# Optimization experiments

Measured on AMD Instinct MI355X. Metric: run time of the kernel, lower is better.

## Reference

```python
import jax, jax.numpy as jnp
import numpy as np

B, S, D, H = 2, 2048, 1024, 16
HD = D // H
SPARSITY = 0.1
LAMBDA_MAX = 10.0
ALPHA = 5.0


def local_prior_mask(seq_len: int, sparsity: float) -> jnp.ndarray:
    # |i - j| <= window_size // 2, window_size = int(seq_len * sparsity)
    window_size = max(1, int(seq_len * sparsity))
    rows = jnp.arange(seq_len)[:, None]
    cols = jnp.arange(seq_len)[None, :]
    return jnp.abs(rows - cols) <= (window_size // 2)


def setup_inputs() -> dict:
    key = jax.random.key(0)
    ks = jax.random.split(key, 12)
    scale = 1.0 / np.sqrt(D)
    inp = {
        'x': jax.random.normal(ks[0], (B, S, D), dtype=jnp.float32),
        'u_prev': jax.random.uniform(ks[1], (B, 1), dtype=jnp.float32),
        'Wq': jax.random.normal(ks[2], (D, D), dtype=jnp.float32) * scale,
        'bq': jnp.zeros((D,), dtype=jnp.float32),
        'Wk': jax.random.normal(ks[3], (D, D), dtype=jnp.float32) * scale,
        'bk': jnp.zeros((D,), dtype=jnp.float32),
        'Wv': jax.random.normal(ks[4], (D, D), dtype=jnp.float32) * scale,
        'bv': jnp.zeros((D,), dtype=jnp.float32),
        'Wo': jax.random.normal(ks[5], (D, D), dtype=jnp.float32) * scale,
        'bo': jnp.zeros((D,), dtype=jnp.float32),
    }
    return inp


def reference(x, u_prev, Wq, bq, Wk, bk, Wv, bv, Wo, bo):
    b, s, _ = x.shape
    # projections (torch Linear: y = x W^T + b)
    def proj(W, bias):
        return (x @ W.T + bias).reshape(b, s, H, HD).transpose(0, 2, 1, 3)  # [B,H,S,HD]
    q = proj(Wq, bq)
    k = proj(Wk, bk)
    v = proj(Wv, bv)

    # dynamic gating: lambda = lambda_max * exp(-alpha * u_prev), shape [B,1,1,1]
    lam = (LAMBDA_MAX * jnp.exp(-ALPHA * u_prev)).reshape(b, 1, 1, 1)

    prior = local_prior_mask(s, SPARSITY)  # [S,S] bool

    scores = jnp.einsum('bhqd,bhkd->bhqk', q, k) / jnp.sqrt(jnp.asarray(HD, x.dtype))
    # additive prior bias: penalize positions outside the structural prior by -lambda
    scores = scores - lam * (~prior).astype(x.dtype)

    attn = jax.nn.softmax(scores, axis=-1)
    out = jnp.einsum('bhqk,bhkd->bhqd', attn, v)           # [B,H,S,HD]
    out = out.transpose(0, 2, 1, 3).reshape(b, s, D)        # [B,S,D]
    out = out @ Wo.T + bo
    return out, lam.reshape(b, 1)
```

## Files before the change

### kernel.cpp

```cpp
#include <hip/hip_runtime.h>

typedef __attribute__((ext_vector_type(8))) short short8;
typedef __attribute__((ext_vector_type(4))) float f32x4;

#define MFMA16(a,b,c) __builtin_amdgcn_mfma_f32_16x16x32_bf16(a,b,c,0,0,0)

__device__ __forceinline__ unsigned short f2bf(float f){
  unsigned int u = __float_as_uint(f);
  u += 0x7FFF + ((u>>16)&1);
  return (unsigned short)(u>>16);
}

__device__ __forceinline__ float fexp2(float x){
#if __has_builtin(__builtin_amdgcn_exp2f)
  return __builtin_amdgcn_exp2f(x);
#else
  return exp2f(x);
#endif
}

__device__ __forceinline__ void gl_lds16(const void* g, void* l){
  __builtin_amdgcn_global_load_lds((const __attribute__((address_space(1))) void*)g,
                                   (__attribute__((address_space(3))) void*)l, 16, 0, 0);
}

__global__ void prep_k(const float* __restrict__ x,
                       const float* __restrict__ Wq, const float* __restrict__ Wk,
                       const float* __restrict__ Wv, const float* __restrict__ Wo,
                       const float* __restrict__ u,
                       unsigned short* __restrict__ xb,
                       unsigned short* __restrict__ Wqkvb,
                       unsigned short* __restrict__ Wob,
                       float* __restrict__ out){
  const int bid = blockIdx.x;
  const float* src;
  unsigned short* dst;
  int lb;
  if (bid < 4096)      { src = x;  dst = xb;              lb = bid; }
  else if (bid < 5120) { src = Wq; dst = Wqkvb;           lb = bid - 4096; }
  else if (bid < 6144) { src = Wk; dst = Wqkvb + 1048576; lb = bid - 5120; }
  else if (bid < 7168) { src = Wv; dst = Wqkvb + 2097152; lb = bid - 6144; }
  else                 { src = Wo; dst = Wob;             lb = bid - 7168; }
  const int i = (lb*256 + threadIdx.x)*4;
  float4 v = *(const float4*)(src + i);
  ushort4 o;
  o.x = f2bf(v.x); o.y = f2bf(v.y); o.z = f2bf(v.z); o.w = f2bf(v.w);
  *(ushort4*)(dst + i) = o;
  if (bid == 0 && threadIdx.x < 2)
    out[4194304 + threadIdx.x] = 10.f*__expf(-5.f*u[threadIdx.x]);
}

__global__ __launch_bounds__(256) void gemm_qkv(
  const unsigned short* __restrict__ A,
  const unsigned short* __restrict__ Bw,
  const float* __restrict__ bias0, const float* __restrict__ bias1, const float* __restrict__ bias2,
  unsigned short* __restrict__ Qo, unsigned short* __restrict__ Ko, unsigned short* __restrict__ VTo,
  int M, int N, int K)
{
  __shared__ unsigned short SM[2][2][128*32];
  unsigned short (*As)[128*32] = SM[0];
  unsigned short (*Bs)[128*32] = SM[1];
  const int tid = threadIdx.x;
  const int nbx = gridDim.x;
  const int lin = blockIdx.x + blockIdx.y*nbx;
  const int cpx = (nbx*gridDim.y) >> 3;
  const int fsw = (lin & 7)*cpx + (lin >> 3);
  const int m0 = (fsw/nbx)*128, n0 = (fsw%nbx)*128;
  const int w = tid>>6, lane = tid&63, lr = lane&15, lg = lane>>4;
  const int wm = w>>1, wn = w&1;
  const int nk = K/32;

  auto stage = [&](int buf, int kt){
    const unsigned short* Ag = A + (size_t)m0*K + kt*32;
    const unsigned short* Bg = Bw + (size_t)n0*K + kt*32;
    #pragma unroll
    for (int it=0; it<2; ++it){
      int slot = it*256 + tid;
      gl_lds16(Ag + (size_t)(slot>>2)*K + (slot&3)*8, &As[buf][slot*8]);
    }
    #pragma unroll
    for (int it=0; it<2; ++it){
      int slot = it*256 + tid;
      gl_lds16(Bg + (size_t)(slot>>2)*K + (slot&3)*8, &Bs[buf][slot*8]);
    }
  };

  f32x4 acc[4][4] = {};
  stage(0,0);
  for (int kt=0; kt<nk; ++kt){
    int cur = kt&1;
    __syncthreads();
    if (kt+1 < nk) stage(cur^1, kt+1);
    short8 af[4], bfr[4];
    #pragma unroll
    for (int i=0;i<4;++i) af[i]  = *(const short8*)&As[cur][(wm*64 + i*16 + lr)*32 + lg*8];
    #pragma unroll
    for (int j=0;j<4;++j) bfr[j] = *(const short8*)&Bs[cur][(wn*64 + j*16 + lr)*32 + lg*8];
    #pragma unroll
    for (int i=0;i<4;++i)
      #pragma unroll
      for (int j=0;j<4;++j)
        acc[i][j] = MFMA16(af[i], bfr[j], acc[i][j]);
  }

  if ((n0>>10)==2){
    unsigned short (*Ct)[136] = (unsigned short(*)[136])&SM[0][0][0];
    const int nb = n0 - 2048;
    #pragma unroll
    for (int hh=0; hh<2; ++hh){
      __syncthreads();
      if (wn == hh){
        #pragma unroll
        for (int i=0;i<4;++i)
          #pragma unroll
          for (int j=0;j<4;++j){
            const int nl = j*16 + lr;
            const float bv = bias2[nb + hh*64 + nl];
            ushort4 pk;
            pk.x = f2bf(acc[i][j][0] + bv);
            pk.y = f2bf(acc[i][j][1] + bv);
            pk.z = f2bf(acc[i][j][2] + bv);
            pk.w = f2bf(acc[i][j][3] + bv);
            *(ushort4*)&Ct[nl][wm*64 + i*16 + lg*4] = pk;
          }
      }
      __syncthreads();
      #pragma unroll
      for (int it=0; it<4; ++it){
        const int idx = it*256 + tid;
        const int nl = idx >> 4, mc = idx & 15;
        short8 vv = *(const short8*)&Ct[nl][mc*8];
        const int nn = nb + hh*64 + nl;
        const int h = nn>>6, hd = nn&63;
        const int mg = m0 + mc*8;
        const int b = mg>>11, s = mg&2047;
        *(short8*)&VTo[((size_t)(b*16 + h)*64 + hd)*2048 + s] = vv;
      }
    }
    return;
  }

  #pragma unroll
  for (int i=0;i<4;++i){
    #pragma unroll
    for (int j=0;j<4;++j){
      const int n  = n0 + wn*64 + j*16 + lr;
      const int mb = m0 + wm*64 + i*16 + lg*4;
      const int which = n>>10, nn = n&1023;
      const float bv = (which==0) ? bias0[nn] : bias1[nn];
      const int h = nn>>6, hd = nn&63;
      #pragma unroll
      for (int r=0;r<4;++r){
        const int m = mb + r;
        const int b = m>>11, s = m&2047;
        const unsigned short u = f2bf(acc[i][j][r] + bv);
        const size_t bh = (size_t)(b*16 + h);
        if (which==0) Qo[(bh*2048 + s)*64 + hd] = u;
        else          Ko[(bh*2048 + s)*64 + hd] = u;
      }
    }
  }
}

__global__ __launch_bounds__(256) void gemm_wo(
  const unsigned short* __restrict__ A,
  const unsigned short* __restrict__ Bw,
  const float* __restrict__ bias0,
  float* __restrict__ Co,
  int M, int N, int K)
{
  __shared__ unsigned short As[2][128*32];
  __shared__ unsigned short Bs[2][64*32];
  const int tid = threadIdx.x;
  const int nbx = gridDim.x;
  const int lin = blockIdx.x + blockIdx.y*nbx;
  const int cpx = (nbx*gridDim.y) >> 3;
  const int fsw = (lin & 7)*cpx + (lin >> 3);
  const int m0 = (fsw/nbx)*128, n0 = (fsw%nbx)*64;
  const int w = tid>>6, lane = tid&63, lr = lane&15, lg = lane>>4;
  const int nk = K/32;

  auto stage = [&](int buf, int kt){
    const unsigned short* Ag = A + (size_t)m0*K + kt*32;
    const unsigned short* Bg = Bw + (size_t)n0*K + kt*32;
    #pragma unroll
    for (int it=0; it<2; ++it){
      int slot = it*256 + tid;
      gl_lds16(Ag + (size_t)(slot>>2)*K + (slot&3)*8, &As[buf][slot*8]);
    }
    gl_lds16(Bg + (size_t)(tid>>2)*K + (tid&3)*8, &Bs[buf][tid*8]);
  };

  f32x4 acc[2][4] = {};
  stage(0,0);
  for (int kt=0; kt<nk; ++kt){
    int cur = kt&1;
    __syncthreads();
    if (kt+1 < nk) stage(cur^1, kt+1);
    short8 af[2], bfr[4];
    #pragma unroll
    for (int i=0;i<2;++i) af[i]  = *(const short8*)&As[cur][(w*32 + i*16 + lr)*32 + lg*8];
    #pragma unroll
    for (int j=0;j<4;++j) bfr[j] = *(const short8*)&Bs[cur][(j*16 + lr)*32 + lg*8];
    #pragma unroll
    for (int i=0;i<2;++i)
      #pragma unroll
      for (int j=0;j<4;++j)
        acc[i][j] = MFMA16(af[i], bfr[j], acc[i][j]);
  }

  #pragma unroll
  for (int i=0;i<2;++i){
    #pragma unroll
    for (int j=0;j<4;++j){
      const int n  = n0 + j*16 + lr;
      const int mb = m0 + w*32 + i*16 + lg*4;
      const float bv = bias0[n];
      #pragma unroll
      for (int r=0;r<4;++r){
        const int m = mb + r;
        Co[(size_t)m*N + n] = acc[i][j][r] + bv;
      }
    }
  }
}

__global__ __launch_bounds__(256, 4) void attn_k(
  const unsigned short* __restrict__ Qb,
  const unsigned short* __restrict__ Kb,
  const unsigned short* __restrict__ VT,
  const float* __restrict__ u_prev,
  unsigned short* __restrict__ Out)
{
  const int lin = blockIdx.x + (blockIdx.y << 5);
  const int f   = ((lin & 7) << 7) + (lin >> 3);
  const int qt  = f & 31, bh = f >> 5;
  const int b = bh>>4, h = bh&15;
  const float lam = 10.f * __expf(-5.f * u_prev[b]);
  const float nlamb = -lam * 1.4426950408889634f;
  const int tid = threadIdx.x;
  const int w = tid>>6, lane = tid&63, lr = lane&15, lg = lane>>4;
  const int q0 = qt*64 + w*16;

  const unsigned short* Qp = Qb + (size_t)bh*2048*64;
  const unsigned short* Kp = Kb + (size_t)bh*2048*64;
  const unsigned short* Vp = VT + (size_t)bh*64*2048;

  __shared__ unsigned short Ks[3][2048];
  __shared__ unsigned short Vs[3][2048];
  __shared__ unsigned short p_lds[4][16][40];

  const unsigned short* ksrc = Kp + (tid&31)*64 + (tid>>5)*8;
  const unsigned short* vsrc = Vp + (size_t)(tid&63)*2048 + (tid>>6)*8;
  unsigned short* kd0 = &Ks[0][tid*8];
  unsigned short* kd1 = &Ks[1][tid*8];
  unsigned short* kd2 = &Ks[2][tid*8];
  unsigned short* vd0 = &Vs[0][tid*8];
  unsigned short* vd1 = &Vs[1][tid*8];
  unsigned short* vd2 = &Vs[2][tid*8];

  const unsigned short* kf0p = &Ks[0][(lg*32+lr)*8];
  const unsigned short* kf1p = &Ks[1][(lg*32+lr)*8];
  const unsigned short* kf2p = &Ks[2][(lg*32+lr)*8];
  const unsigned short* vf0p = &Vs[0][(lg*64+lr)*8];
  const unsigned short* vf1p = &Vs[1][(lg*64+lr)*8];
  const unsigned short* vf2p = &Vs[2][(lg*64+lr)*8];
  const unsigned short* pap  = &p_lds[w][lr][lg*8];
  unsigned short* pwp = &p_lds[w][lg*4][lr];

  short8 qf0 = *(const short8*)&Qp[(size_t)(q0+lr)*64 +      lg*8];
  short8 qf1 = *(const short8*)&Qp[(size_t)(q0+lr)*64 + 32 + lg*8];

  const float c1 = 0.18033688011112042f;
  float l_run[4] = {0.f, 0.f, 0.f, 0.f};
  f32x4 o0 = {}, o1 = {}, o2 = {}, o3 = {};
  const f32x4 zf = {};
  f32x4 sA0, sA1, sB0, sB1, sC0, sC1;

#define STAGE_(KD, VD, KT) do{ const int kw_ = (KT)&63; \
    gl_lds16(ksrc + ((size_t)kw_<<11), (KD)); \
    gl_lds16(vsrc + (kw_<<5), (VD)); }while(0)

#define BAR_ do{ \
    asm volatile("s_waitcnt vmcnt(2) lgkmcnt(0)\n\ts_barrier" ::: "memory"); \
    __builtin_amdgcn_sched_barrier(0); }while(0)

#define QKM_(KP, S0, S1) do{ \
    short8 ka_ = *(const short8*)(KP); \
    short8 kb_ = *(const short8*)((KP)+1024); \
    short8 kc_ = *(const short8*)((KP)+128); \
    short8 kd_ = *(const short8*)((KP)+1152); \
    S0 = MFMA16(qf0, ka_, zf); S0 = MFMA16(qf1, kb_, S0); \
    S1 = MFMA16(qf0, kc_, zf); S1 = MFMA16(qf1, kd_, S1); }while(0)

#define SOFT_(KT, SIN0, SIN1) do{ \
    const int k0_ = (KT)*32; \
    const int cls_ = (k0_ > q0 + 117 || k0_ < q0 - 133) ? 2 \
                   : (k0_ >= q0 - 87 && k0_ <= q0 + 71) ? 0 : 1; \
    _Pragma("unroll") \
    for (int r=0;r<4;++r){ \
      const int qi_ = q0 + lg*4 + r; \
      float b0 = 0.f, b1 = 0.f; \
      if (cls_ == 2){ b0 = nlamb; b1 = nlamb; } \
      else if (cls_ == 1){ \
        int d0 = qi_ - (k0_ + lr);      if (d0<0) d0 = -d0; \
        int d1 = qi_ - (k0_ + 16 + lr); if (d1<0) d1 = -d1; \
        if (d0 > 102) b0 = nlamb; \
        if (d1 > 102) b1 = nlamb; \
      } \
      const float p0 = fexp2(fmaf((SIN0)[r], c1, b0)); \
      const float p1 = fexp2(fmaf((SIN1)[r], c1, b1)); \
      l_run[r] += p0 + p1; \
      pwp[r*40]      = (unsigned short)(__float_as_uint(p0)>>16); \
      pwp[r*40 + 16] = (unsigned short)(__float_as_uint(p1)>>16); \
    } }while(0)

#define BODY_(KT, VFPC, KDC, VDC, KFPN, SIN0, SIN1, SOUT0, SOUT1) do{ \
    SOFT_((KT), SIN0, SIN1); \
    short8 vfa_ = *(const short8*)(VFPC); \
    short8 vfb_ = *(const short8*)((VFPC)+128); \
    short8 vfc_ = *(const short8*)((VFPC)+256); \
    short8 vfd_ = *(const short8*)((VFPC)+384); \
    short8 pa_  = *(const short8*)(pap); \
    BAR_; \
    STAGE_((KDC), (VDC), (KT)+3); \
    QKM_((KFPN), SOUT0, SOUT1); \
    o0 = MFMA16(pa_, vfa_, o0); \
    o1 = MFMA16(pa_, vfb_, o1); \
    o2 = MFMA16(pa_, vfc_, o2); \
    o3 = MFMA16(pa_, vfd_, o3); }while(0)

  STAGE_(kd0, vd0, 0);
  STAGE_(kd1, vd1, 1);
  STAGE_(kd2, vd2, 2);
  BAR_;
  QKM_(kf0p, sA0, sA1);

  for (int it=0; it<21; ++it){
    const int kt = it*3;
    BODY_(kt,   vf0p, kd0, vd0, kf1p, sA0, sA1, sB0, sB1);
    BODY_(kt+1, vf1p, kd1, vd1, kf2p, sB0, sB1, sC0, sC1);
    BODY_(kt+2, vf2p, kd2, vd2, kf0p, sC0, sC1, sA0, sA1);
  }
  {
    SOFT_(63, sA0, sA1);
    short8 vfa_ = *(const short8*)(vf0p);
    short8 vfb_ = *(const short8*)(vf0p+128);
    short8 vfc_ = *(const short8*)(vf0p+256);
    short8 vfd_ = *(const short8*)(vf0p+384);
    asm volatile("s_waitcnt lgkmcnt(0)" ::: "memory");
    __builtin_amdgcn_sched_barrier(0);
    short8 pa_  = *(const short8*)(pap);
    o0 = MFMA16(pa_, vfa_, o0);
    o1 = MFMA16(pa_, vfb_, o1);
    o2 = MFMA16(pa_, vfc_, o2);
    o3 = MFMA16(pa_, vfd_, o3);
  }
#undef BODY_
#undef SOFT_
#undef QKM_
#undef BAR_
#undef STAGE_

  #pragma unroll
  for (int off=1; off<16; off<<=1)
    #pragma unroll
    for (int r=0;r<4;++r)
      l_run[r] += __shfl_xor(l_run[r], off, 64);

  #pragma unroll
  for (int r=0;r<4;++r){
    const int qi = q0 + lg*4 + r;
    const float linv = 1.0f / l_run[r];
    unsigned short* op = &Out[((size_t)b*2048 + qi)*1024 + h*64 + lr];
    op[0]  = f2bf(o0[r] * linv);
    op[16] = f2bf(o1[r] * linv);
    op[32] = f2bf(o2[r] * linv);
    op[48] = f2bf(o3[r] * linv);
  }
}

extern "C" void kernel_launch(void* const* d_in, const int* in_sizes, int n_in,
                              void* d_out, int out_size, void* d_ws, size_t ws_size,
                              hipStream_t stream){
  const float* x  = (const float*)d_in[0];
  const float* u  = (const float*)d_in[1];
  const float* Wq = (const float*)d_in[2];
  const float* bq = (const float*)d_in[3];
  const float* Wk = (const float*)d_in[4];
  const float* bk = (const float*)d_in[5];
  const float* Wv = (const float*)d_in[6];
  const float* bv = (const float*)d_in[7];
  const float* Wo = (const float*)d_in[8];
  const float* bo = (const float*)d_in[9];
  float* out = (float*)d_out;

  unsigned char* ws = (unsigned char*)d_ws;
  unsigned short* xb    = (unsigned short*)(ws);
  unsigned short* attnb = xb;
  unsigned short* Wqkvb = (unsigned short*)(ws + 8388608);
  unsigned short* Wob   = (unsigned short*)(ws + 14680064);
  unsigned short* Qb2   = (unsigned short*)(ws + 16777216);
  unsigned short* Kb2   = (unsigned short*)(ws + 25165824);
  unsigned short* VTb   = (unsigned short*)(ws + 33554432);

  prep_k<<<8192, 256, 0, stream>>>(x, Wq, Wk, Wv, Wo, u, xb, Wqkvb, Wob, out);

  gemm_qkv<<<dim3(24,32), 256, 0, stream>>>(xb, Wqkvb, bq, bk, bv,
                                            Qb2, Kb2, VTb, 4096, 3072, 1024);
  attn_k<<<dim3(32,32), 256, 0, stream>>>(Qb2, Kb2, VTb, u, attnb);
  gemm_wo<<<dim3(16,32), 256, 0, stream>>>(attnb, Wob, bo, out, 4096, 1024, 1024);
}
```

Baseline: 140.3 us.

## Split attention KV range in halves and merge partials in a combine kernel

The attention kernel now splits each (batch, head, query tile) over two halves of the key/value sequence, doubling the block count. Each block writes unnormalized bf16 partial outputs and row sums, and a new combine kernel adds the two halves, normalizes, and writes the head-interleaved layout. The LDS pipeline shrinks from three stages to two with plain __syncthreads, and launch bounds allow more blocks per CU. This buys more parallelism and occupancy at the cost of an extra launch, extra global traffic for the partials, and a less deeply overlapped load pipeline.

```diff
diff --git a/kernel.cpp b/kernel.cpp
--- a/kernel.cpp
+++ b/kernel.cpp
@@ -9,6 +9,10 @@
   unsigned int u = __float_as_uint(f);
   u += 0x7FFF + ((u>>16)&1);
   return (unsigned short)(u>>16);
+}
+
+__device__ __forceinline__ float bf2f(unsigned short u){
+  return __uint_as_float(((unsigned int)u)<<16);
 }
 
 __device__ __forceinline__ float fexp2(float x){
@@ -225,17 +229,19 @@
   }
 }
 
-__global__ __launch_bounds__(256, 4) void attn_k(
+__global__ __launch_bounds__(256, 7) void attn_k(
   const unsigned short* __restrict__ Qb,
   const unsigned short* __restrict__ Kb,
   const unsigned short* __restrict__ VT,
   const float* __restrict__ u_prev,
-  unsigned short* __restrict__ Out)
+  unsigned short* __restrict__ opart,
+  float* __restrict__ lpart)
 {
-  const int lin = blockIdx.x + (blockIdx.y << 5);
-  const int f   = ((lin & 7) << 7) + (lin >> 3);
-  const int qt  = f & 31, bh = f >> 5;
-  const int b = bh>>4, h = bh&15;
+  const int lin = blockIdx.x + (blockIdx.y << 6);
+  const int f   = ((lin & 7) << 8) + (lin >> 3);
+  const int qt  = f & 31, half = (f >> 5) & 1, bh = f >> 6;
+  const int kv0 = half*32;
+  const int b = bh>>4;
   const float lam = 10.f * __expf(-5.f * u_prev[b]);
   const float nlamb = -lam * 1.4426950408889634f;
   const int tid = threadIdx.x;
@@ -246,25 +252,21 @@
   const unsigned short* Kp = Kb + (size_t)bh*2048*64;
   const unsigned short* Vp = VT + (size_t)bh*64*2048;
 
-  __shared__ unsigned short Ks[3][2048];
-  __shared__ unsigned short Vs[3][2048];
+  __shared__ unsigned short Ks[2][2048];
+  __shared__ unsigned short Vs[2][2048];
   __shared__ unsigned short p_lds[4][16][40];
 
   const unsigned short* ksrc = Kp + (tid&31)*64 + (tid>>5)*8;
   const unsigned short* vsrc = Vp + (size_t)(tid&63)*2048 + (tid>>6)*8;
   unsigned short* kd0 = &Ks[0][tid*8];
   unsigned short* kd1 = &Ks[1][tid*8];
-  unsigned short* kd2 = &Ks[2][tid*8];
   unsigned short* vd0 = &Vs[0][tid*8];
   unsigned short* vd1 = &Vs[1][tid*8];
-  unsigned short* vd2 = &Vs[2][tid*8];
 
   const unsigned short* kf0p = &Ks[0][(lg*32+lr)*8];
   const unsigned short* kf1p = &Ks[1][(lg*32+lr)*8];
-  const unsigned short* kf2p = &Ks[2][(lg*32+lr)*8];
   const unsigned short* vf0p = &Vs[0][(lg*64+lr)*8];
   const unsigned short* vf1p = &Vs[1][(lg*64+lr)*8];
-  const unsigned short* vf2p = &Vs[2][(lg*64+lr)*8];
   const unsigned short* pap  = &p_lds[w][lr][lg*8];
   unsigned short* pwp = &p_lds[w][lg*4][lr];
 
@@ -275,15 +277,11 @@
   float l_run[4] = {0.f, 0.f, 0.f, 0.f};
   f32x4 o0 = {}, o1 = {}, o2 = {}, o3 = {};
   const f32x4 zf = {};
-  f32x4 sA0, sA1, sB0, sB1, sC0, sC1;
+  f32x4 s0, s1, t0, t1;
 
 #define STAGE_(KD, VD, KT) do{ const int kw_ = (KT)&63; \
     gl_lds16(ksrc + ((size_t)kw_<<11), (KD)); \
     gl_lds16(vsrc + (kw_<<5), (VD)); }while(0)
-
-#define BAR_ do{ \
-    asm volatile("s_waitcnt vmcnt(2) lgkmcnt(0)\n\ts_barrier" ::: "memory"); \
-    __builtin_amdgcn_sched_barrier(0); }while(0)
 
 #define QKM_(KP, S0, S1) do{ \
     short8 ka_ = *(const short8*)(KP); \
@@ -293,7 +291,7 @@
     S0 = MFMA16(qf0, ka_, zf); S0 = MFMA16(qf1, kb_, S0); \
     S1 = MFMA16(qf0, kc_, zf); S1 = MFMA16(qf1, kd_, S1); }while(0)
 
-#define SOFT_(KT, SIN0, SIN1) do{ \
+#define BODY_(KT, VFPC, KDC, VDC, KFPN, SIN0, SIN1, SOUT0, SOUT1) do{ \
     const int k0_ = (KT)*32; \
     const int cls_ = (k0_ > q0 + 117 || k0_ < q0 - 133) ? 2 \
                    : (k0_ >= q0 - 87 && k0_ <= q0 + 71) ? 0 : 1; \
@@ -313,53 +311,34 @@
       l_run[r] += p0 + p1; \
       pwp[r*40]      = (unsigned short)(__float_as_uint(p0)>>16); \
       pwp[r*40 + 16] = (unsigned short)(__float_as_uint(p1)>>16); \
-    } }while(0)
-
-#define BODY_(KT, VFPC, KDC, VDC, KFPN, SIN0, SIN1, SOUT0, SOUT1) do{ \
-    SOFT_((KT), SIN0, SIN1); \
+    } \
     short8 vfa_ = *(const short8*)(VFPC); \
     short8 vfb_ = *(const short8*)((VFPC)+128); \
     short8 vfc_ = *(const short8*)((VFPC)+256); \
     short8 vfd_ = *(const short8*)((VFPC)+384); \
     short8 pa_  = *(const short8*)(pap); \
-    BAR_; \
-    STAGE_((KDC), (VDC), (KT)+3); \
+    __syncthreads(); \
+    STAGE_((KDC), (VDC), (KT)+2); \
+    f32x4 SOUT0 = zf, SOUT1 = zf; \
     QKM_((KFPN), SOUT0, SOUT1); \
     o0 = MFMA16(pa_, vfa_, o0); \
     o1 = MFMA16(pa_, vfb_, o1); \
     o2 = MFMA16(pa_, vfc_, o2); \
-    o3 = MFMA16(pa_, vfd_, o3); }while(0)
-
-  STAGE_(kd0, vd0, 0);
-  STAGE_(kd1, vd1, 1);
-  STAGE_(kd2, vd2, 2);
-  BAR_;
-  QKM_(kf0p, sA0, sA1);
-
-  for (int it=0; it<21; ++it){
-    const int kt = it*3;
-    BODY_(kt,   vf0p, kd0, vd0, kf1p, sA0, sA1, sB0, sB1);
-    BODY_(kt+1, vf1p, kd1, vd1, kf2p, sB0, sB1, sC0, sC1);
-    BODY_(kt+2, vf2p, kd2, vd2, kf0p, sC0, sC1, sA0, sA1);
-  }
-  {
-    SOFT_(63, sA0, sA1);
-    short8 vfa_ = *(const short8*)(vf0p);
-    short8 vfb_ = *(const short8*)(vf0p+128);
-    short8 vfc_ = *(const short8*)(vf0p+256);
-    short8 vfd_ = *(const short8*)(vf0p+384);
-    asm volatile("s_waitcnt lgkmcnt(0)" ::: "memory");
-    __builtin_amdgcn_sched_barrier(0);
-    short8 pa_  = *(const short8*)(pap);
-    o0 = MFMA16(pa_, vfa_, o0);
-    o1 = MFMA16(pa_, vfb_, o1);
-    o2 = MFMA16(pa_, vfc_, o2);
-    o3 = MFMA16(pa_, vfd_, o3);
+    o3 = MFMA16(pa_, vfd_, o3); \
+    SIN0 = SOUT0; SIN1 = SOUT1; }while(0)
+
+  STAGE_(kd0, vd0, kv0);
+  __syncthreads();
+  STAGE_(kd1, vd1, kv0+1);
+  QKM_(kf0p, s0, s1);
+
+  for (int it=0; it<16; ++it){
+    const int kt = kv0 + 2*it;
+    BODY_(kt,   vf0p, kd0, vd0, kf1p, s0, s1, u0_, u1_);
+    BODY_(kt+1, vf1p, kd1, vd1, kf0p, s0, s1, u2_, u3_);
   }
 #undef BODY_
-#undef SOFT_
 #undef QKM_
-#undef BAR_
 #undef STAGE_
 
   #pragma unroll
@@ -368,16 +347,36 @@
     for (int r=0;r<4;++r)
       l_run[r] += __shfl_xor(l_run[r], off, 64);
 
+  unsigned short* po = opart + ((size_t)(half*32 + bh)*2048)*64;
   #pragma unroll
   for (int r=0;r<4;++r){
     const int qi = q0 + lg*4 + r;
-    const float linv = 1.0f / l_run[r];
-    unsigned short* op = &Out[((size_t)b*2048 + qi)*1024 + h*64 + lr];
-    op[0]  = f2bf(o0[r] * linv);
-    op[16] = f2bf(o1[r] * linv);
-    op[32] = f2bf(o2[r] * linv);
-    op[48] = f2bf(o3[r] * linv);
-  }
+    unsigned short* op = po + (size_t)qi*64 + lr;
+    op[0]  = f2bf(o0[r]);
+    op[16] = f2bf(o1[r]);
+    op[32] = f2bf(o2[r]);
+    op[48] = f2bf(o3[r]);
+    if (lr == 0) lpart[(size_t)(half*32 + bh)*2048 + qi] = l_run[r];
+  }
+}
+
+__global__ void combine_k(const unsigned short* __restrict__ opart,
+                          const float* __restrict__ lpart,
+                          unsigned short* __restrict__ attnb){
+  const int idx = blockIdx.x*256 + threadIdx.x;
+  const int rowq = idx >> 3, seg = idx & 7;
+  short8 a = *(const short8*)&opart[(size_t)rowq*64 + seg*8];
+  short8 c = *(const short8*)&opart[(size_t)(65536 + rowq)*64 + seg*8];
+  const float linv = 1.f/(lpart[rowq] + lpart[65536 + rowq]);
+  const int bh = rowq >> 11, q = rowq & 2047;
+  const int b = bh >> 4, h = bh & 15;
+  short8 wv;
+  #pragma unroll
+  for (int e=0;e<8;++e){
+    const float o = (bf2f((unsigned short)a[e]) + bf2f((unsigned short)c[e])) * linv;
+    wv[e] = (short)f2bf(o);
+  }
+  *(short8*)&attnb[((size_t)(b*2048 + q))*1024 + h*64 + seg*8] = wv;
 }
 
 extern "C" void kernel_launch(void* const* d_in, const int* in_sizes, int n_in,
@@ -403,11 +402,14 @@
   unsigned short* Qb2   = (unsigned short*)(ws + 16777216);
   unsigned short* Kb2   = (unsigned short*)(ws + 25165824);
   unsigned short* VTb   = (unsigned short*)(ws + 33554432);
+  float*          lpart = (float*)(ws + 8388608);
+  unsigned short* opart = (unsigned short*)d_out;
 
   prep_k<<<8192, 256, 0, stream>>>(x, Wq, Wk, Wv, Wo, u, xb, Wqkvb, Wob, out);
 
   gemm_qkv<<<dim3(24,32), 256, 0, stream>>>(xb, Wqkvb, bq, bk, bv,
                                             Qb2, Kb2, VTb, 4096, 3072, 1024);
-  attn_k<<<dim3(32,32), 256, 0, stream>>>(Qb2, Kb2, VTb, u, attnb);
+  attn_k<<<dim3(64,32), 256, 0, stream>>>(Qb2, Kb2, VTb, u, opart, lpart);
+  combine_k<<<2048, 256, 0, stream>>>(opart, lpart, attnb);
   gemm_wo<<<dim3(16,32), 256, 0, stream>>>(attnb, Wob, bo, out, 4096, 1024, 1024);
 }
```

New measurement: 318.6 us. 127% more time.
